# Kernel optimization log

Hardware: AMD Instinct MI355X
Metric: run time of the kernel (lower is better)

Reference implementation:

```python
import jax, jax.numpy as jnp
import numpy as np

D = 512      # input_dim
H = 128      # hidden_dim
K = max(32, int(D * 0.7))  # output_dim = 358
B = 65536    # batch


def setup_inputs() -> dict:
    key = jax.random.key(0)
    ks = jax.random.split(key, 16)
    s = lambda fan_in: 1.0 / np.sqrt(fan_in)
    inp = {
        "x": jax.random.normal(ks[0], (B, D), dtype=jnp.float32),
        # importance net: D->H->H->D, sigmoid
        "W1": jax.random.uniform(ks[1], (D, H), minval=-s(D), maxval=s(D)),
        "b1": jnp.zeros((H,), jnp.float32),
        "W2": jax.random.uniform(ks[2], (H, H), minval=-s(H), maxval=s(H)),
        "b2": jnp.zeros((H,), jnp.float32),
        "W3": jax.random.uniform(ks[3], (H, D), minval=-s(H), maxval=s(H)),
        "b3": jnp.zeros((D,), jnp.float32),
        # gate net: D->H->D, sigmoid
        "Wg1": jax.random.uniform(ks[4], (D, H), minval=-s(D), maxval=s(D)),
        "bg1": jnp.zeros((H,), jnp.float32),
        "Wg2": jax.random.uniform(ks[5], (H, D), minval=-s(H), maxval=s(H)),
        "bg2": jnp.zeros((D,), jnp.float32),
        # reconstruction net: D->H->K
        "Wr1": jax.random.uniform(ks[6], (D, H), minval=-s(D), maxval=s(D)),
        "br1": jnp.zeros((H,), jnp.float32),
        "Wr2": jax.random.uniform(ks[7], (H, K), minval=-s(H), maxval=s(H)),
        "br2": jnp.zeros((K,), jnp.float32),
    }
    return inp


def reference(x, W1, b1, W2, b2, W3, b3, Wg1, bg1, Wg2, bg2, Wr1, br1, Wr2, br2):
    # importance scores: sigmoid MLP D->H->H->D
    h = jax.nn.relu(x @ W1 + b1)
    h = jax.nn.relu(h @ W2 + b2)
    importance = jax.nn.sigmoid(h @ W3 + b3)            # [B, D]
    # attention gate: sigmoid MLP D->H->D
    g = jax.nn.relu(x @ Wg1 + bg1)
    gate = jax.nn.sigmoid(g @ Wg2 + bg2)                # [B, D]
    combined = importance * gate                        # [B, D]
    # top-k feature mask (scatter 1.0 at topk indices)
    _, idx = jax.lax.top_k(combined, K)                 # [B, K]
    rows = jnp.arange(combined.shape[0])[:, None]
    mask = jnp.zeros_like(combined).at[rows, idx].set(1.0)
    masked = x * mask                                   # [B, D]
    # reconstruction MLP D->H->K
    r = jax.nn.relu(masked @ Wr1 + br1)
    selected = r @ Wr2 + br2                            # [B, K]
    # AdaptiveFeatureSelector.forward returns only selected features
    return selected
```

## Files before the change

### kernel.cpp

```cpp
#include <hip/hip_runtime.h>
#include <math.h>

#define BD 512
#define HH 128
#define KSEL 358
#define TR 16
#define NT 512
#define XP 4
#define HP 4

typedef __attribute__((ext_vector_type(8))) short bf16x8;
typedef __attribute__((ext_vector_type(4))) float f32x4;

__device__ __forceinline__ float cephes_expf(float x) {
    x = fminf(x, 88.3762626647950f);
    x = fmaxf(x, -88.3762626647949f);
    float m = floorf(fmaf(x, 1.44269504088896341f, 0.5f));
    float r = __fsub_rn(x, __fmul_rn(m, 0.693359375f));
    r = __fsub_rn(r, __fmul_rn(m, -2.12194440e-4f));
    float r2 = __fmul_rn(r, r);
    float p = 1.9875691500E-4f;
    p = fmaf(p, r, 1.3981999507E-3f);
    p = fmaf(p, r, 8.3334519073E-3f);
    p = fmaf(p, r, 4.1665795894E-2f);
    p = fmaf(p, r, 1.6666665459E-1f);
    p = fmaf(p, r, 5.0000001201E-1f);
    float y = __fadd_rn(fmaf(p, r2, r), 1.0f);
    int mi = (int)m;
    y = __int_as_float(__float_as_int(y) + (mi << 23));
    return y;
}

__device__ __forceinline__ float sig_xla(float z) {
    float t = cephes_expf(-z);
    float d = __fadd_rn(1.0f, t);
    return __fdiv_rn(1.0f, d);
}

__device__ __forceinline__ void split8t(const float* v, bf16x8& hi, bf16x8& lo) {
    #pragma unroll
    for (int s = 0; s < 8; ++s) {
        unsigned u = __float_as_uint(v[s]);
        float hf = __uint_as_float(u & 0xffff0000u);
        float res = v[s] - hf;
        hi[s] = (short)(u >> 16);
        lo[s] = (short)(__float_as_uint(res) >> 16);
    }
}

__global__ void presplit(const float* __restrict__ Wr1, const float* __restrict__ Wr2,
                         unsigned short* __restrict__ w1h, unsigned short* __restrict__ w1l,
                         unsigned short* __restrict__ w2h, unsigned short* __restrict__ w2l)
{
    const int i = blockIdx.x * blockDim.x + threadIdx.x;
    if (i < BD * HH) {
        float v = Wr1[i];
        unsigned u = __float_as_uint(v);
        w1h[i] = (unsigned short)(u >> 16);
        float res = v - __uint_as_float(u & 0xffff0000u);
        w1l[i] = (unsigned short)(__float_as_uint(res) >> 16);
    }
    if (i < HH * KSEL) {
        float v = Wr2[i];
        unsigned u = __float_as_uint(v);
        w2h[i] = (unsigned short)(u >> 16);
        float res = v - __uint_as_float(u & 0xffff0000u);
        w2l[i] = (unsigned short)(__float_as_uint(res) >> 16);
    }
}

__global__ __launch_bounds__(NT, 4)
void afs_fused(const float* __restrict__ x,
               const float* __restrict__ W1,  const float* __restrict__ b1,
               const float* __restrict__ W2,  const float* __restrict__ b2,
               const float* __restrict__ W3,  const float* __restrict__ b3,
               const float* __restrict__ Wg1, const float* __restrict__ bg1,
               const float* __restrict__ Wg2, const float* __restrict__ bg2,
               const float* __restrict__ br1,
               const float* __restrict__ br2,
               const unsigned short* __restrict__ w1h, const unsigned short* __restrict__ w1l,
               const unsigned short* __restrict__ w2h, const unsigned short* __restrict__ w2l,
               float* __restrict__ out)
{
    __shared__ float xs[TR][BD + XP];
    __shared__ float h1s[TR][HH + HP];
    __shared__ float cs[TR][BD];

    float* h2f = &cs[0][0];
    float* g1f = &cs[0][0] + TR * HH;
    float (*rs)[HH + HP] = h1s;

    const int tid = threadIdx.x;
    const long long row0 = (long long)blockIdx.x * TR;

    {
        #pragma unroll
        for (int i = tid; i < TR * (BD / 4); i += NT) {
            const int r = i >> 7;
            const int c4 = (i & 127) * 4;
            *reinterpret_cast<float4*>(&xs[r][c4]) =
                *reinterpret_cast<const float4*>(&x[(row0 + r) * BD + c4]);
        }
    }
    __syncthreads();

    {
        const int c = tid & (HH - 1);
        const int rbase = (tid >> 7) * 4;
        const float* __restrict__ pw1 = W1 + c;
        const float* __restrict__ pwg = Wg1 + c;
        float a1[4] = {0.f, 0.f, 0.f, 0.f};
        float ga[4] = {0.f, 0.f, 0.f, 0.f};
        for (int k0 = 0; k0 < BD; k0 += 8) {
            float xq[4][8];
            #pragma unroll
            for (int r = 0; r < 4; ++r) {
                *reinterpret_cast<float4*>(&xq[r][0]) =
                    *reinterpret_cast<const float4*>(&xs[rbase + r][k0]);
                *reinterpret_cast<float4*>(&xq[r][4]) =
                    *reinterpret_cast<const float4*>(&xs[rbase + r][k0 + 4]);
            }
            #pragma unroll
            for (int kk = 0; kk < 8; ++kk) {
                const float w1 = pw1[kk * HH];
                const float wg = pwg[kk * HH];
                #pragma unroll
                for (int r = 0; r < 4; ++r) {
                    a1[r] = fmaf(xq[r][kk], w1, a1[r]);
                    ga[r] = fmaf(xq[r][kk], wg, ga[r]);
                }
            }
            pw1 += 8 * HH;
            pwg += 8 * HH;
        }
        float bb1 = b1[c], bbg = bg1[c];
        #pragma unroll
        for (int r = 0; r < 4; ++r) {
            float v1 = __fadd_rn(a1[r], bb1);
            float vg = __fadd_rn(ga[r], bbg);
            h1s[rbase + r][c] = v1 > 0.f ? v1 : 0.f;
            g1f[(rbase + r) * HH + c] = vg > 0.f ? vg : 0.f;
        }
    }
    __syncthreads();

    {
        const int c = tid & (HH - 1);
        const int rbase = (tid >> 7) * 4;
        const float* __restrict__ pw = W2 + c;
        float acc[4] = {0.f, 0.f, 0.f, 0.f};
        for (int k0 = 0; k0 < HH; k0 += 8) {
            float hq[4][8];
            #pragma unroll
            for (int r = 0; r < 4; ++r) {
                *reinterpret_cast<float4*>(&hq[r][0]) =
                    *reinterpret_cast<const float4*>(&h1s[rbase + r][k0]);
                *reinterpret_cast<float4*>(&hq[r][4]) =
                    *reinterpret_cast<const float4*>(&h1s[rbase + r][k0 + 4]);
            }
            #pragma unroll
            for (int kk = 0; kk < 8; ++kk) {
                const float w = pw[kk * HH];
                #pragma unroll
                for (int r = 0; r < 4; ++r)
                    acc[r] = fmaf(hq[r][kk], w, acc[r]);
            }
            pw += 8 * HH;
        }
        float bb = b2[c];
        #pragma unroll
        for (int r = 0; r < 4; ++r) {
            float v = __fadd_rn(acc[r], bb);
            h2f[(rbase + r) * HH + c] = v > 0.f ? v : 0.f;
        }
    }
    __syncthreads();

    {
        const int c = tid;
        float zi[TR], zg[TR];
        #pragma unroll
        for (int r = 0; r < TR; ++r) zi[r] = 0.f;
        {
            const float* __restrict__ pw = W3 + c;
            for (int k0 = 0; k0 < HH; k0 += 4) {
                float wv[4];
                #pragma unroll
                for (int kk = 0; kk < 4; ++kk) wv[kk] = pw[kk * BD];
                float hq[8][4];
                #pragma unroll
                for (int r = 0; r < 8; ++r)
                    *reinterpret_cast<float4*>(&hq[r][0]) =
                        *reinterpret_cast<const float4*>(&h2f[r * HH + k0]);
                #pragma unroll
                for (int kk = 0; kk < 4; ++kk)
                    #pragma unroll
                    for (int r = 0; r < 8; ++r)
                        zi[r] = fmaf(hq[r][kk], wv[kk], zi[r]);
                #pragma unroll
                for (int r = 0; r < 8; ++r)
                    *reinterpret_cast<float4*>(&hq[r][0]) =
                        *reinterpret_cast<const float4*>(&h2f[(8 + r) * HH + k0]);
                #pragma unroll
                for (int kk = 0; kk < 4; ++kk)
                    #pragma unroll
                    for (int r = 0; r < 8; ++r)
                        zi[8 + r] = fmaf(hq[r][kk], wv[kk], zi[8 + r]);
                pw += 4 * BD;
            }
        }
        #pragma unroll
        for (int r = 0; r < TR; ++r) zg[r] = 0.f;
        {
            const float* __restrict__ pw = Wg2 + c;
            for (int k0 = 0; k0 < HH; k0 += 4) {
                float wv[4];
                #pragma unroll
                for (int kk = 0; kk < 4; ++kk) wv[kk] = pw[kk * BD];
                float gq[8][4];
                #pragma unroll
                for (int r = 0; r < 8; ++r)
                    *reinterpret_cast<float4*>(&gq[r][0]) =
                        *reinterpret_cast<const float4*>(&g1f[r * HH + k0]);
                #pragma unroll
                for (int kk = 0; kk < 4; ++kk)
                    #pragma unroll
                    for (int r = 0; r < 8; ++r)
                        zg[r] = fmaf(gq[r][kk], wv[kk], zg[r]);
                #pragma unroll
                for (int r = 0; r < 8; ++r)
                    *reinterpret_cast<float4*>(&gq[r][0]) =
                        *reinterpret_cast<const float4*>(&g1f[(8 + r) * HH + k0]);
                #pragma unroll
                for (int kk = 0; kk < 4; ++kk)
                    #pragma unroll
                    for (int r = 0; r < 8; ++r)
                        zg[8 + r] = fmaf(gq[r][kk], wv[kk], zg[8 + r]);
                pw += 4 * BD;
            }
        }
        __syncthreads();
        float bi = b3[c];
        float bq = bg2[c];
        #pragma unroll
        for (int r = 0; r < TR; ++r) {
            cs[r][c] = __fmul_rn(sig_xla(__fadd_rn(zi[r], bi)),
                                 sig_xla(__fadd_rn(zg[r], bq)));
        }
    }
    __syncthreads();

    {
        const int lane = tid & 63;
        const int wv = tid >> 6;
        for (int rr = 0; rr < 2; ++rr) {
            const int r = wv + rr * 8;
            unsigned u[8];
            #pragma unroll
            for (int j = 0; j < 8; ++j)
                u[j] = __float_as_uint(cs[r][j * 64 + lane]);

            unsigned lo = 0u, hi = 0x3F800000u;
            while (lo < hi) {
                unsigned mid = lo + ((hi - lo) >> 1);
                int cnt = 0;
                #pragma unroll
                for (int j = 0; j < 8; ++j)
                    cnt += __popcll(__ballot(u[j] > mid));
                if (cnt < KSEL) hi = mid; else lo = mid + 1;
            }
            const unsigned T = lo;

            int ngt = 0, neq = 0;
            #pragma unroll
            for (int j = 0; j < 8; ++j) {
                ngt += __popcll(__ballot(u[j] > T));
                neq += __popcll(__ballot(u[j] == T));
            }
            const int m = KSEL - ngt;

            unsigned selbits = 0;
            #pragma unroll
            for (int j = 0; j < 8; ++j)
                if (u[j] > T) selbits |= (1u << j);

            if (neq == m) {
                #pragma unroll
                for (int j = 0; j < 8; ++j)
                    if (u[j] == T) selbits |= (1u << j);
            } else {
                int cnt8[8];
                #pragma unroll
                for (int j = 0; j < 8; ++j) cnt8[j] = 0;
                for (int jj = 0; jj < BD; ++jj) {
                    unsigned uj = __float_as_uint(cs[r][jj]);
                    if (uj == T) {
                        #pragma unroll
                        for (int j = 0; j < 8; ++j)
                            cnt8[j] += (u[j] == T && jj < (j * 64 + lane)) ? 1 : 0;
                    }
                }
                #pragma unroll
                for (int j = 0; j < 8; ++j)
                    if (u[j] == T && (ngt + cnt8[j]) < KSEL)
                        selbits |= (1u << j);
            }

            #pragma unroll
            for (int j = 0; j < 8; ++j)
                if (!(selbits & (1u << j))) xs[r][j * 64 + lane] = 0.0f;
        }
    }
    __syncthreads();

    {
        const int lane = tid & 63;
        const int w = tid >> 6;
        const int arow = lane & 15;
        const int kb = (lane >> 4) * 8;
        const int j0 = w * 16;
        const int col = lane & 15;
        f32x4 acc = {0.f, 0.f, 0.f, 0.f};
        const unsigned short* __restrict__ pBh = w1h + j0 + col;
        const unsigned short* __restrict__ pBl = w1l + j0 + col;
        #pragma unroll 2
        for (int kt = 0; kt < 16; ++kt) {
            const int k0 = kt * 32 + kb;
            float av[8];
            *reinterpret_cast<float4*>(&av[0]) =
                *reinterpret_cast<const float4*>(&xs[arow][k0]);
            *reinterpret_cast<float4*>(&av[4]) =
                *reinterpret_cast<const float4*>(&xs[arow][k0 + 4]);
            bf16x8 ah, al;
            split8t(av, ah, al);
            bf16x8 bh, bl;
            #pragma unroll
            for (int s = 0; s < 8; ++s) {
                bh[s] = (short)pBh[(k0 + s) * HH];
                bl[s] = (short)pBl[(k0 + s) * HH];
            }
            acc = __builtin_amdgcn_mfma_f32_16x16x32_bf16(ah, bh, acc, 0, 0, 0);
            acc = __builtin_amdgcn_mfma_f32_16x16x32_bf16(ah, bl, acc, 0, 0, 0);
            acc = __builtin_amdgcn_mfma_f32_16x16x32_bf16(al, bh, acc, 0, 0, 0);
        }
        float bias = br1[j0 + col];
        #pragma unroll
        for (int reg = 0; reg < 4; ++reg) {
            const int rr = (lane >> 4) * 4 + reg;
            float v = acc[reg] + bias;
            rs[rr][j0 + col] = v > 0.f ? v : 0.f;
        }
    }
    __syncthreads();

    {
        const int lane = tid & 63;
        const int w = tid >> 6;
        const int arow = lane & 15;
        const int kb = (lane >> 4) * 8;
        const int col = lane & 15;
        bf16x8 ah[4], al[4];
        #pragma unroll
        for (int kt = 0; kt < 4; ++kt) {
            const int k0 = kt * 32 + kb;
            float av[8];
            *reinterpret_cast<float4*>(&av[0]) =
                *reinterpret_cast<const float4*>(&rs[arow][k0]);
            *reinterpret_cast<float4*>(&av[4]) =
                *reinterpret_cast<const float4*>(&rs[arow][k0 + 4]);
            split8t(av, ah[kt], al[kt]);
        }
        for (int jt = w; jt < 23; jt += 8) {
            const int j0 = jt * 16;
            const int cc = j0 + col;
            const bool ok = (cc < KSEL);
            f32x4 acc = {0.f, 0.f, 0.f, 0.f};
            #pragma unroll
            for (int kt = 0; kt < 4; ++kt) {
                const int k0 = kt * 32 + kb;
                bf16x8 bh, bl;
                #pragma unroll
                for (int s = 0; s < 8; ++s) {
                    bh[s] = ok ? (short)w2h[(k0 + s) * KSEL + cc] : (short)0;
                    bl[s] = ok ? (short)w2l[(k0 + s) * KSEL + cc] : (short)0;
                }
                acc = __builtin_amdgcn_mfma_f32_16x16x32_bf16(ah[kt], bh, acc, 0, 0, 0);
                acc = __builtin_amdgcn_mfma_f32_16x16x32_bf16(ah[kt], bl, acc, 0, 0, 0);
                acc = __builtin_amdgcn_mfma_f32_16x16x32_bf16(al[kt], bh, acc, 0, 0, 0);
            }
            if (ok) {
                float bias = br2[cc];
                #pragma unroll
                for (int reg = 0; reg < 4; ++reg) {
                    const int rr = (lane >> 4) * 4 + reg;
                    out[(row0 + rr) * KSEL + cc] = acc[reg] + bias;
                }
            }
        }
    }
}

extern "C" void kernel_launch(void* const* d_in, const int* in_sizes, int n_in,
                              void* d_out, int out_size, void* d_ws, size_t ws_size,
                              hipStream_t stream) {
    const float* x   = (const float*)d_in[0];
    const float* W1  = (const float*)d_in[1];
    const float* b1  = (const float*)d_in[2];
    const float* W2  = (const float*)d_in[3];
    const float* b2  = (const float*)d_in[4];
    const float* W3  = (const float*)d_in[5];
    const float* b3  = (const float*)d_in[6];
    const float* Wg1 = (const float*)d_in[7];
    const float* bg1 = (const float*)d_in[8];
    const float* Wg2 = (const float*)d_in[9];
    const float* bg2 = (const float*)d_in[10];
    const float* Wr1 = (const float*)d_in[11];
    const float* br1 = (const float*)d_in[12];
    const float* Wr2 = (const float*)d_in[13];
    const float* br2 = (const float*)d_in[14];
    float* out = (float*)d_out;

    unsigned short* w1h = (unsigned short*)d_ws;
    unsigned short* w1l = w1h + BD * HH;
    unsigned short* w2h = w1l + BD * HH;
    unsigned short* w2l = w2h + HH * KSEL;

    presplit<<<dim3((BD * HH + 255) / 256), dim3(256), 0, stream>>>(
        Wr1, Wr2, w1h, w1l, w2h, w2l);

    const int nrows = in_sizes[0] / BD;
    dim3 grid(nrows / TR), block(NT);
    afs_fused<<<grid, block, 0, stream>>>(x, W1, b1, W2, b2, W3, b3,
                                          Wg1, bg1, Wg2, bg2, br1, br2,
                                          w1h, w1l, w2h, w2l, out);
}
```

Before: 859.3 us.

## Prepack reconstruction weights into MFMA fragment layout and pre-split activations in LDS

The reconstruction weights are now repacked once into the per-lane bf16x8 fragment order used by the MFMA instructions, so each lane loads a B fragment with one vector load instead of eight strided scalar loads. The masked input and the hidden activations are split into bf16 hi/lo halves once when written to shared memory, which removes the repeated split work in the GEMM loops. The masked x row is re-read from global memory at the point of masking, which adds some global traffic.

```diff
diff --git a/kernel.cpp b/kernel.cpp
--- a/kernel.cpp
+++ b/kernel.cpp
@@ -8,6 +8,13 @@
 #define NT 512
 #define XP 4
 #define HP 4
+
+#define XSU_STRIDE ((BD + XP) * 2)
+#define XL_OFF 520
+#define RS_STRIDE ((HH + HP) * 2)
+#define RSL_OFF 136
+
+#define P2N (23 * 4 * 64 * 8)
 
 typedef __attribute__((ext_vector_type(8))) short bf16x8;
 typedef __attribute__((ext_vector_type(4))) float f32x4;
@@ -37,35 +44,40 @@
     return __fdiv_rn(1.0f, d);
 }
 
-__device__ __forceinline__ void split8t(const float* v, bf16x8& hi, bf16x8& lo) {
-    #pragma unroll
-    for (int s = 0; s < 8; ++s) {
-        unsigned u = __float_as_uint(v[s]);
-        float hf = __uint_as_float(u & 0xffff0000u);
-        float res = v[s] - hf;
-        hi[s] = (short)(u >> 16);
-        lo[s] = (short)(__float_as_uint(res) >> 16);
-    }
-}
-
-__global__ void presplit(const float* __restrict__ Wr1, const float* __restrict__ Wr2,
-                         unsigned short* __restrict__ w1h, unsigned short* __restrict__ w1l,
-                         unsigned short* __restrict__ w2h, unsigned short* __restrict__ w2l)
+__global__ void prepack(const float* __restrict__ Wr1, const float* __restrict__ Wr2,
+                        unsigned short* __restrict__ p1h, unsigned short* __restrict__ p1l,
+                        unsigned short* __restrict__ p2h, unsigned short* __restrict__ p2l)
 {
-    const int i = blockIdx.x * blockDim.x + threadIdx.x;
-    if (i < BD * HH) {
-        float v = Wr1[i];
-        unsigned u = __float_as_uint(v);
-        w1h[i] = (unsigned short)(u >> 16);
-        float res = v - __uint_as_float(u & 0xffff0000u);
-        w1l[i] = (unsigned short)(__float_as_uint(res) >> 16);
-    }
-    if (i < HH * KSEL) {
-        float v = Wr2[i];
-        unsigned u = __float_as_uint(v);
-        w2h[i] = (unsigned short)(u >> 16);
-        float res = v - __uint_as_float(u & 0xffff0000u);
-        w2l[i] = (unsigned short)(__float_as_uint(res) >> 16);
+    const int t = blockIdx.x * blockDim.x + threadIdx.x;
+    if (t < 8 * 16 * 64) {
+        const int jb = t >> 10, kt = (t >> 6) & 15, lane = t & 63;
+        const int col = lane & 15, kg = lane >> 4;
+        const int base = t * 8;
+        #pragma unroll
+        for (int s = 0; s < 8; ++s) {
+            const int k = kt * 32 + kg * 8 + s;
+            float v = Wr1[k * HH + jb * 16 + col];
+            unsigned u = __float_as_uint(v);
+            p1h[base + s] = (unsigned short)(u >> 16);
+            float res = v - __uint_as_float(u & 0xffff0000u);
+            p1l[base + s] = (unsigned short)(__float_as_uint(res) >> 16);
+        }
+    }
+    const int t2 = t - 8 * 16 * 64;
+    if (t2 >= 0 && t2 < 23 * 4 * 64) {
+        const int jt = t2 >> 8, kt = (t2 >> 6) & 3, lane = t2 & 63;
+        const int col = lane & 15, kg = lane >> 4;
+        const int cg = jt * 16 + col;
+        const int base = t2 * 8;
+        #pragma unroll
+        for (int s = 0; s < 8; ++s) {
+            const int k = kt * 32 + kg * 8 + s;
+            float v = (cg < KSEL) ? Wr2[k * KSEL + cg] : 0.f;
+            unsigned u = __float_as_uint(v);
+            p2h[base + s] = (unsigned short)(u >> 16);
+            float res = v - __uint_as_float(u & 0xffff0000u);
+            p2l[base + s] = (unsigned short)(__float_as_uint(res) >> 16);
+        }
     }
 }
 
@@ -78,8 +90,8 @@
                const float* __restrict__ Wg2, const float* __restrict__ bg2,
                const float* __restrict__ br1,
                const float* __restrict__ br2,
-               const unsigned short* __restrict__ w1h, const unsigned short* __restrict__ w1l,
-               const unsigned short* __restrict__ w2h, const unsigned short* __restrict__ w2l,
+               const unsigned short* __restrict__ p1h, const unsigned short* __restrict__ p1l,
+               const unsigned short* __restrict__ p2h, const unsigned short* __restrict__ p2l,
                float* __restrict__ out)
 {
     __shared__ float xs[TR][BD + XP];
@@ -88,7 +100,6 @@
 
     float* h2f = &cs[0][0];
     float* g1f = &cs[0][0] + TR * HH;
-    float (*rs)[HH + HP] = h1s;
 
     const int tid = threadIdx.x;
     const long long row0 = (long long)blockIdx.x * TR;
@@ -253,8 +264,14 @@
     {
         const int lane = tid & 63;
         const int wv = tid >> 6;
+        unsigned short* xsu = (unsigned short*)&xs[0][0];
         for (int rr = 0; rr < 2; ++rr) {
             const int r = wv + rr * 8;
+            const float* __restrict__ pxr = x + (row0 + r) * BD;
+            float xr[8];
+            #pragma unroll
+            for (int j = 0; j < 8; ++j) xr[j] = pxr[j * 64 + lane];
+
             unsigned u[8];
             #pragma unroll
             for (int j = 0; j < 8; ++j)
@@ -307,8 +324,15 @@
             }
 
             #pragma unroll
-            for (int j = 0; j < 8; ++j)
-                if (!(selbits & (1u << j))) xs[r][j * 64 + lane] = 0.0f;
+            for (int j = 0; j < 8; ++j) {
+                const int d = j * 64 + lane;
+                float v = (selbits & (1u << j)) ? xr[j] : 0.0f;
+                unsigned uu = __float_as_uint(v);
+                float res = v - __uint_as_float(uu & 0xffff0000u);
+                xsu[r * XSU_STRIDE + d] = (unsigned short)(uu >> 16);
+                xsu[r * XSU_STRIDE + XL_OFF + d] =
+                    (unsigned short)(__float_as_uint(res) >> 16);
+            }
         }
     }
     __syncthreads();
@@ -320,35 +344,33 @@
         const int kb = (lane >> 4) * 8;
         const int j0 = w * 16;
         const int col = lane & 15;
+        const unsigned short* xsu = (const unsigned short*)&xs[0][0];
+        const bf16x8* pBh = reinterpret_cast<const bf16x8*>(p1h) + w * 16 * 64 + lane;
+        const bf16x8* pBl = reinterpret_cast<const bf16x8*>(p1l) + w * 16 * 64 + lane;
         f32x4 acc = {0.f, 0.f, 0.f, 0.f};
-        const unsigned short* __restrict__ pBh = w1h + j0 + col;
-        const unsigned short* __restrict__ pBl = w1l + j0 + col;
         #pragma unroll 2
         for (int kt = 0; kt < 16; ++kt) {
             const int k0 = kt * 32 + kb;
-            float av[8];
-            *reinterpret_cast<float4*>(&av[0]) =
-                *reinterpret_cast<const float4*>(&xs[arow][k0]);
-            *reinterpret_cast<float4*>(&av[4]) =
-                *reinterpret_cast<const float4*>(&xs[arow][k0 + 4]);
-            bf16x8 ah, al;
-            split8t(av, ah, al);
-            bf16x8 bh, bl;
-            #pragma unroll
-            for (int s = 0; s < 8; ++s) {
-                bh[s] = (short)pBh[(k0 + s) * HH];
-                bl[s] = (short)pBl[(k0 + s) * HH];
-            }
+            bf16x8 ah = *reinterpret_cast<const bf16x8*>(&xsu[arow * XSU_STRIDE + k0]);
+            bf16x8 al = *reinterpret_cast<const bf16x8*>(&xsu[arow * XSU_STRIDE + XL_OFF + k0]);
+            bf16x8 bh = pBh[kt * 64];
+            bf16x8 bl = pBl[kt * 64];
             acc = __builtin_amdgcn_mfma_f32_16x16x32_bf16(ah, bh, acc, 0, 0, 0);
             acc = __builtin_amdgcn_mfma_f32_16x16x32_bf16(ah, bl, acc, 0, 0, 0);
             acc = __builtin_amdgcn_mfma_f32_16x16x32_bf16(al, bh, acc, 0, 0, 0);
         }
         float bias = br1[j0 + col];
+        unsigned short* rsu = (unsigned short*)&h1s[0][0];
         #pragma unroll
         for (int reg = 0; reg < 4; ++reg) {
             const int rr = (lane >> 4) * 4 + reg;
             float v = acc[reg] + bias;
-            rs[rr][j0 + col] = v > 0.f ? v : 0.f;
+            v = v > 0.f ? v : 0.f;
+            unsigned uu = __float_as_uint(v);
+            float res = v - __uint_as_float(uu & 0xffff0000u);
+            rsu[rr * RS_STRIDE + j0 + col] = (unsigned short)(uu >> 16);
+            rsu[rr * RS_STRIDE + RSL_OFF + j0 + col] =
+                (unsigned short)(__float_as_uint(res) >> 16);
         }
     }
     __syncthreads();
@@ -359,36 +381,28 @@
         const int arow = lane & 15;
         const int kb = (lane >> 4) * 8;
         const int col = lane & 15;
+        const unsigned short* rsu = (const unsigned short*)&h1s[0][0];
         bf16x8 ah[4], al[4];
         #pragma unroll
         for (int kt = 0; kt < 4; ++kt) {
             const int k0 = kt * 32 + kb;
-            float av[8];
-            *reinterpret_cast<float4*>(&av[0]) =
-                *reinterpret_cast<const float4*>(&rs[arow][k0]);
-            *reinterpret_cast<float4*>(&av[4]) =
-                *reinterpret_cast<const float4*>(&rs[arow][k0 + 4]);
-            split8t(av, ah[kt], al[kt]);
+            ah[kt] = *reinterpret_cast<const bf16x8*>(&rsu[arow * RS_STRIDE + k0]);
+            al[kt] = *reinterpret_cast<const bf16x8*>(&rsu[arow * RS_STRIDE + RSL_OFF + k0]);
         }
         for (int jt = w; jt < 23; jt += 8) {
-            const int j0 = jt * 16;
-            const int cc = j0 + col;
-            const bool ok = (cc < KSEL);
+            const int cc = jt * 16 + col;
+            const bf16x8* pBh = reinterpret_cast<const bf16x8*>(p2h) + jt * 4 * 64 + lane;
+            const bf16x8* pBl = reinterpret_cast<const bf16x8*>(p2l) + jt * 4 * 64 + lane;
             f32x4 acc = {0.f, 0.f, 0.f, 0.f};
             #pragma unroll
             for (int kt = 0; kt < 4; ++kt) {
-                const int k0 = kt * 32 + kb;
-                bf16x8 bh, bl;
-                #pragma unroll
-                for (int s = 0; s < 8; ++s) {
-                    bh[s] = ok ? (short)w2h[(k0 + s) * KSEL + cc] : (short)0;
-                    bl[s] = ok ? (short)w2l[(k0 + s) * KSEL + cc] : (short)0;
-                }
+                bf16x8 bh = pBh[kt * 64];
+                bf16x8 bl = pBl[kt * 64];
                 acc = __builtin_amdgcn_mfma_f32_16x16x32_bf16(ah[kt], bh, acc, 0, 0, 0);
                 acc = __builtin_amdgcn_mfma_f32_16x16x32_bf16(ah[kt], bl, acc, 0, 0, 0);
                 acc = __builtin_amdgcn_mfma_f32_16x16x32_bf16(al[kt], bh, acc, 0, 0, 0);
             }
-            if (ok) {
+            if (cc < KSEL) {
                 float bias = br2[cc];
                 #pragma unroll
                 for (int reg = 0; reg < 4; ++reg) {
@@ -420,17 +434,18 @@
     const float* br2 = (const float*)d_in[14];
     float* out = (float*)d_out;
 
-    unsigned short* w1h = (unsigned short*)d_ws;
-    unsigned short* w1l = w1h + BD * HH;
-    unsigned short* w2h = w1l + BD * HH;
-    unsigned short* w2l = w2h + HH * KSEL;
-
-    presplit<<<dim3((BD * HH + 255) / 256), dim3(256), 0, stream>>>(
-        Wr1, Wr2, w1h, w1l, w2h, w2l);
+    unsigned short* p1h = (unsigned short*)d_ws;
+    unsigned short* p1l = p1h + BD * HH;
+    unsigned short* p2h = p1l + BD * HH;
+    unsigned short* p2l = p2h + P2N;
+
+    const int npack = 8 * 16 * 64 + 23 * 4 * 64;
+    prepack<<<dim3((npack + 255) / 256), dim3(256), 0, stream>>>(
+        Wr1, Wr2, p1h, p1l, p2h, p2l);
 
     const int nrows = in_sizes[0] / BD;
     dim3 grid(nrows / TR), block(NT);
     afs_fused<<<grid, block, 0, stream>>>(x, W1, b1, W2, b2, W3, b3,
                                           Wg1, bg1, Wg2, bg2, br1, br2,
-                                          w1h, w1l, w2h, w2l, out);
+                                          p1h, p1l, p2h, p2l, out);
 }
```

New measurement: 810.2 us. -5.7%, faster.
